# Optimization experiments

Hardware: AMD Instinct MI355X
Metric: run time of the kernel (lower is better)

The kernel has to match this reference:

```python
import jax, jax.numpy as jnp
import numpy as np

S = 64.0
M = 0.5
EPS = 1e-07
NORM_EPS = 1e-12  # matches torch F.normalize default eps
B, D, C = 512, 512, 64000


def _l2_normalize(a, axis=-1):
    n = jnp.sqrt(jnp.sum(a * a, axis=axis, keepdims=True))
    return a / jnp.maximum(n, NORM_EPS)


def setup_inputs() -> dict:
    key = jax.random.key(0)
    kx, ky, kw = jax.random.split(key, 3)
    x = jax.random.normal(kx, (B, D), dtype=jnp.float32)
    y = jax.random.randint(ky, (B,), 0, C, dtype=jnp.int64)
    # kaiming_uniform-ish init: bound = sqrt(6 / fan_in)
    bound = np.sqrt(6.0 / D).astype(np.float32)
    W = jax.random.uniform(kw, (C, D), dtype=jnp.float32, minval=-bound, maxval=bound)
    return {"x": x, "y": y, "W": W}


def reference(x, y, W):
    # cosine similarities: [B, C]
    theta = _l2_normalize(x) @ _l2_normalize(W).T
    # target logit per row
    tgt = jnp.take_along_axis(theta, y[:, None], axis=1)[:, 0]  # [B]
    numerator = S * jnp.cos(jnp.arccos(jnp.clip(tgt, -1.0 + EPS, 1.0 - EPS)) + M)
    # sum of exp(s*theta) over non-target classes (mask out target column)
    is_tgt = jnp.arange(C, dtype=y.dtype)[None, :] == y[:, None]  # [B, C]
    excl_sum = jnp.sum(jnp.where(is_tgt, 0.0, jnp.exp(S * theta)), axis=1)  # [B]
    denominator = jnp.exp(numerator) + excl_sum
    return -jnp.mean(numerator - jnp.log(denominator))
```

## Files before the change

### kernel.cpp

```cpp
#include <hip/hip_runtime.h>


#define B_N 512
#define D_N 512
#define C_N 64000
#define S_SCALE 64.0f
#define MARGIN 0.5f
#define EPS_C 1e-7f

typedef unsigned short ushort_t;
typedef __attribute__((ext_vector_type(8))) short short8;
typedef __attribute__((ext_vector_type(4))) float floatx4;

__device__ __forceinline__ ushort_t f2bf(float f) {
    unsigned int u = __float_as_uint(f);
    u += 0x7fffu + ((u >> 16) & 1u);
    return (ushort_t)(u >> 16);
}

__global__ void prep_kernel(const float* __restrict__ W,
                            const float* __restrict__ x,
                            ushort_t* __restrict__ Wn,
                            ushort_t* __restrict__ xn,
                            float* __restrict__ rowsum) {
    int b = blockIdx.x;
    int t = threadIdx.x;
    if (b == 16128) {
        rowsum[t] = 0.0f;
        rowsum[t + 256] = 0.0f;
        return;
    }
    const float* src;
    ushort_t* dst;
    int row;
    if (b < 16000) {
        row = b * 4 + (t >> 6);
        src = W + (size_t)row * D_N;
        dst = Wn + (size_t)row * D_N;
    } else {
        row = (b - 16000) * 4 + (t >> 6);
        src = x + (size_t)row * D_N;
        dst = xn + (size_t)row * D_N;
    }
    int lane = t & 63;
    const float4* p = (const float4*)src;
    float4 v0 = p[lane];
    float4 v1 = p[lane + 64];
    float ss = v0.x*v0.x + v0.y*v0.y + v0.z*v0.z + v0.w*v0.w
             + v1.x*v1.x + v1.y*v1.y + v1.z*v1.z + v1.w*v1.w;
#pragma unroll
    for (int off = 32; off > 0; off >>= 1) ss += __shfl_xor(ss, off);
    float sc = 1.0f / fmaxf(sqrtf(ss), 1e-12f);
    uint2 o0, o1;
    o0.x = (unsigned)f2bf(v0.x*sc) | ((unsigned)f2bf(v0.y*sc) << 16);
    o0.y = (unsigned)f2bf(v0.z*sc) | ((unsigned)f2bf(v0.w*sc) << 16);
    o1.x = (unsigned)f2bf(v1.x*sc) | ((unsigned)f2bf(v1.y*sc) << 16);
    o1.y = (unsigned)f2bf(v1.z*sc) | ((unsigned)f2bf(v1.w*sc) << 16);
    *(uint2*)(dst + lane * 4)       = o0;
    *(uint2*)(dst + 256 + lane * 4) = o1;
}

__device__ __forceinline__ void g2lds16(const ushort_t* g, ushort_t* l) {
    __builtin_amdgcn_global_load_lds(
        (const __attribute__((address_space(1))) void*)g,
        (__attribute__((address_space(3))) void*)l, 16, 0, 0);
}

__global__ void gemm_arcface_kernel(const ushort_t* __restrict__ A,
                                    const ushort_t* __restrict__ Bm,
                                    const int* __restrict__ y,
                                    float* __restrict__ rowsum,
                                    float* __restrict__ tgt) {
    __shared__ ushort_t sA[2 * 128 * 32];
    __shared__ ushort_t sB[2 * 128 * 32];
    __shared__ float rowacc[128];

    int t    = threadIdx.x;
    int lane = t & 63;
    int w    = t >> 6;
    int wr   = w >> 1, wc = w & 1;
    int rm0  = blockIdx.x * 128;
    int cn0  = blockIdx.y * 128;

    if (t < 128) rowacc[t] = 0.0f;

    floatx4 acc[4][4];
#pragma unroll
    for (int i = 0; i < 4; i++)
#pragma unroll
        for (int j = 0; j < 4; j++) acc[i][j] = (floatx4){0.f, 0.f, 0.f, 0.f};

    const ushort_t* gA0 = A  + (size_t)(rm0 + (t >> 2)) * D_N + (t & 3) * 8;
    const ushort_t* gB0 = Bm + (size_t)(cn0 + (t >> 2)) * D_N + (t & 3) * 8;

    int lq = lane >> 4;
    int lc = lane & 15;
    int fragA_off = (wr * 64 + lc) * 32 + lq * 8;
    int fragB_off = (wc * 64 + lc) * 32 + lq * 8;

    g2lds16(gA0,            sA + t * 8);
    g2lds16(gA0 + 64 * D_N, sA + (t + 256) * 8);
    g2lds16(gB0,            sB + t * 8);
    g2lds16(gB0 + 64 * D_N, sB + (t + 256) * 8);
    __syncthreads();

    for (int k = 0; k < 16; ++k) {
        int cur = (k & 1) * 4096;
        if (k < 15) {
            int nxt = ((k + 1) & 1) * 4096;
            int kk  = (k + 1) * 32;
            g2lds16(gA0 + kk,            sA + nxt + t * 8);
            g2lds16(gA0 + 64 * D_N + kk, sA + nxt + (t + 256) * 8);
            g2lds16(gB0 + kk,            sB + nxt + t * 8);
            g2lds16(gB0 + 64 * D_N + kk, sB + nxt + (t + 256) * 8);
        }

        short8 af[4], bf[4];
#pragma unroll
        for (int tm = 0; tm < 4; tm++)
            af[tm] = *(const short8*)(sA + cur + fragA_off + tm * 512);
#pragma unroll
        for (int tn = 0; tn < 4; tn++)
            bf[tn] = *(const short8*)(sB + cur + fragB_off + tn * 512);
#pragma unroll
        for (int tm = 0; tm < 4; tm++)
#pragma unroll
            for (int tn = 0; tn < 4; tn++)
                acc[tm][tn] = __builtin_amdgcn_mfma_f32_16x16x32_bf16(
                    af[tm], bf[tn], acc[tm][tn], 0, 0, 0);
        __syncthreads();
    }

#pragma unroll
    for (int tm = 0; tm < 4; tm++) {
#pragma unroll
        for (int r = 0; r < 4; r++) {
            int lrow = wr * 64 + tm * 16 + lq * 4 + r;
            int grow = rm0 + lrow;
            int yv   = y[grow];
            float esum = 0.0f;
#pragma unroll
            for (int tn = 0; tn < 4; tn++) {
                int gcol = cn0 + wc * 64 + tn * 16 + lc;
                float theta = acc[tm][tn][r];
                if (gcol == yv) {
                    tgt[grow] = theta;
                } else {
                    esum += __expf(S_SCALE * theta);
                }
            }
#pragma unroll
            for (int off = 1; off < 16; off <<= 1) esum += __shfl_xor(esum, off);
            if (lc == 0) atomicAdd(&rowacc[lrow], esum);
        }
    }
    __syncthreads();
    if (t < 128) atomicAdd(&rowsum[rm0 + t], rowacc[t]);
}

__global__ void finalize_kernel(const float* __restrict__ rowsum,
                                const float* __restrict__ tgt,
                                float* __restrict__ out) {
    __shared__ float red[256];
    int t = threadIdx.x;
    float s = 0.0f;
    for (int r = t; r < B_N; r += 256) {
        float tv = tgt[r];
        tv = fminf(fmaxf(tv, -1.0f + EPS_C), 1.0f - EPS_C);
        float num = S_SCALE * cosf(acosf(tv) + MARGIN);
        float den = expf(num) + rowsum[r];
        s += num - logf(den);
    }
    red[t] = s;
    __syncthreads();
    for (int o = 128; o > 0; o >>= 1) {
        if (t < o) red[t] += red[t + o];
        __syncthreads();
    }
    if (t == 0) out[0] = -red[0] / (float)B_N;
}

extern "C" void kernel_launch(void* const* d_in, const int* in_sizes, int n_in,
                              void* d_out, int out_size, void* d_ws, size_t ws_size,
                              hipStream_t stream) {
    const float* x = (const float*)d_in[0];
    const int*   y = (const int*)d_in[1];
    const float* W = (const float*)d_in[2];
    float* out = (float*)d_out;

    char* ws = (char*)d_ws;
    ushort_t* xn = (ushort_t*)ws;
    ushort_t* Wn = (ushort_t*)(ws + 524288);
    float* rowsum = (float*)(ws + 524288 + (size_t)C_N * D_N * 2);
    float* tgt    = rowsum + B_N;

    prep_kernel<<<16129, 256, 0, stream>>>(W, x, Wn, xn, rowsum);
    dim3 grid(4, C_N / 128);
    gemm_arcface_kernel<<<grid, 256, 0, stream>>>(xn, Wn, y, rowsum, tgt);
    finalize_kernel<<<1, 256, 0, stream>>>(rowsum, tgt, out);
}
```

Baseline: 256.0 us.

## Fuse W normalization into GEMM with full-K W tile resident in LDS

W row normalization and bf16 conversion now happen inside the GEMM kernel. Each 512-thread block normalizes 64 W rows into a swizzled LDS buffer covering the full K dimension, then streams all 512 normalized x rows against them. This removes the 64 MB bf16 Wn write and re-read and the separate large prep pass over W, leaving a single fp32 read of W. In exchange each block uses roughly 128 KB of LDS, which lowers occupancy, and shared x tiles are re-streamed from L2 by every block.

Result: slower. 269.4 us (+5.2%).

```diff
diff --git a/kernel.cpp b/kernel.cpp
--- a/kernel.cpp
+++ b/kernel.cpp
@@ -18,32 +18,19 @@
     return (ushort_t)(u >> 16);
 }
 
-__global__ void prep_kernel(const float* __restrict__ W,
-                            const float* __restrict__ x,
-                            ushort_t* __restrict__ Wn,
-                            ushort_t* __restrict__ xn,
-                            float* __restrict__ rowsum) {
+__global__ void xprep_kernel(const float* __restrict__ x,
+                             ushort_t* __restrict__ xn,
+                             float* __restrict__ rowsum) {
     int b = blockIdx.x;
     int t = threadIdx.x;
-    if (b == 16128) {
+    if (b == 128) {
         rowsum[t] = 0.0f;
         rowsum[t + 256] = 0.0f;
         return;
     }
-    const float* src;
-    ushort_t* dst;
-    int row;
-    if (b < 16000) {
-        row = b * 4 + (t >> 6);
-        src = W + (size_t)row * D_N;
-        dst = Wn + (size_t)row * D_N;
-    } else {
-        row = (b - 16000) * 4 + (t >> 6);
-        src = x + (size_t)row * D_N;
-        dst = xn + (size_t)row * D_N;
-    }
+    int row  = b * 4 + (t >> 6);
     int lane = t & 63;
-    const float4* p = (const float4*)src;
+    const float4* p = (const float4*)(x + (size_t)row * D_N);
     float4 v0 = p[lane];
     float4 v1 = p[lane + 64];
     float ss = v0.x*v0.x + v0.y*v0.y + v0.z*v0.z + v0.w*v0.w
@@ -51,6 +38,7 @@
 #pragma unroll
     for (int off = 32; off > 0; off >>= 1) ss += __shfl_xor(ss, off);
     float sc = 1.0f / fmaxf(sqrtf(ss), 1e-12f);
+    ushort_t* dst = xn + (size_t)row * D_N;
     uint2 o0, o1;
     o0.x = (unsigned)f2bf(v0.x*sc) | ((unsigned)f2bf(v0.y*sc) << 16);
     o0.y = (unsigned)f2bf(v0.z*sc) | ((unsigned)f2bf(v0.w*sc) << 16);
@@ -66,23 +54,48 @@
         (__attribute__((address_space(3))) void*)l, 16, 0, 0);
 }
 
-__global__ void gemm_arcface_kernel(const ushort_t* __restrict__ A,
-                                    const ushort_t* __restrict__ Bm,
-                                    const int* __restrict__ y,
-                                    float* __restrict__ rowsum,
-                                    float* __restrict__ tgt) {
-    __shared__ ushort_t sA[2 * 128 * 32];
-    __shared__ ushort_t sB[2 * 128 * 32];
-    __shared__ float rowacc[128];
+__global__ __launch_bounds__(512, 2)
+void gemm_fused_kernel(const float* __restrict__ W,
+                       const ushort_t* __restrict__ xn,
+                       const int* __restrict__ y,
+                       float* __restrict__ rowsum,
+                       float* __restrict__ tgt) {
+    __shared__ ushort_t sW[64 * 512];
+    __shared__ ushort_t sA[2 * 512 * 32];
 
     int t    = threadIdx.x;
     int lane = t & 63;
     int w    = t >> 6;
-    int wr   = w >> 1, wc = w & 1;
-    int rm0  = blockIdx.x * 128;
-    int cn0  = blockIdx.y * 128;
-
-    if (t < 128) rowacc[t] = 0.0f;
+    int lq   = lane >> 4;
+    int lc   = lane & 15;
+    int cn0  = blockIdx.x * 64;
+
+#pragma unroll
+    for (int rr = 0; rr < 8; ++rr) {
+        int row = w * 8 + rr;
+        const float4* p = (const float4*)(W + (size_t)(cn0 + row) * D_N);
+        float4 a = p[lane * 2];
+        float4 b = p[lane * 2 + 1];
+        float ss = a.x*a.x + a.y*a.y + a.z*a.z + a.w*a.w
+                 + b.x*b.x + b.y*b.y + b.z*b.z + b.w*b.w;
+#pragma unroll
+        for (int off = 32; off > 0; off >>= 1) ss += __shfl_xor(ss, off);
+        float sc = 1.0f / fmaxf(sqrtf(ss), 1e-12f);
+        uint4 o;
+        o.x = (unsigned)f2bf(a.x*sc) | ((unsigned)f2bf(a.y*sc) << 16);
+        o.y = (unsigned)f2bf(a.z*sc) | ((unsigned)f2bf(a.w*sc) << 16);
+        o.z = (unsigned)f2bf(b.x*sc) | ((unsigned)f2bf(b.y*sc) << 16);
+        o.w = (unsigned)f2bf(b.z*sc) | ((unsigned)f2bf(b.w*sc) << 16);
+        int kc = lane;
+        int rs = row ^ (kc & 7);
+        *((uint4*)(sW + kc * 512 + rs * 8)) = o;
+    }
+
+    const ushort_t* gA = xn + (size_t)(t >> 2) * D_N + (t & 3) * 8;
+#pragma unroll
+    for (int c = 0; c < 4; ++c)
+        g2lds16(gA + (size_t)c * 128 * D_N, sA + (t + c * 512) * 8);
+    __syncthreads();
 
     floatx4 acc[4][4];
 #pragma unroll
@@ -90,72 +103,62 @@
 #pragma unroll
         for (int j = 0; j < 4; j++) acc[i][j] = (floatx4){0.f, 0.f, 0.f, 0.f};
 
-    const ushort_t* gA0 = A  + (size_t)(rm0 + (t >> 2)) * D_N + (t & 3) * 8;
-    const ushort_t* gB0 = Bm + (size_t)(cn0 + (t >> 2)) * D_N + (t & 3) * 8;
-
-    int lq = lane >> 4;
-    int lc = lane & 15;
-    int fragA_off = (wr * 64 + lc) * 32 + lq * 8;
-    int fragB_off = (wc * 64 + lc) * 32 + lq * 8;
-
-    g2lds16(gA0,            sA + t * 8);
-    g2lds16(gA0 + 64 * D_N, sA + (t + 256) * 8);
-    g2lds16(gB0,            sB + t * 8);
-    g2lds16(gB0 + 64 * D_N, sB + (t + 256) * 8);
-    __syncthreads();
+    int fragA_base = (w * 64 + lc) * 32 + lq * 8;
 
     for (int k = 0; k < 16; ++k) {
-        int cur = (k & 1) * 4096;
+        int cur = (k & 1) * 16384;
         if (k < 15) {
-            int nxt = ((k + 1) & 1) * 4096;
+            int nxt = ((k + 1) & 1) * 16384;
             int kk  = (k + 1) * 32;
-            g2lds16(gA0 + kk,            sA + nxt + t * 8);
-            g2lds16(gA0 + 64 * D_N + kk, sA + nxt + (t + 256) * 8);
-            g2lds16(gB0 + kk,            sB + nxt + t * 8);
-            g2lds16(gB0 + 64 * D_N + kk, sB + nxt + (t + 256) * 8);
+#pragma unroll
+            for (int c = 0; c < 4; ++c)
+                g2lds16(gA + (size_t)c * 128 * D_N + kk,
+                        sA + nxt + (t + c * 512) * 8);
         }
-
-        short8 af[4], bf[4];
+        short8 af[4], bfr[4];
 #pragma unroll
         for (int tm = 0; tm < 4; tm++)
-            af[tm] = *(const short8*)(sA + cur + fragA_off + tm * 512);
-#pragma unroll
-        for (int tn = 0; tn < 4; tn++)
-            bf[tn] = *(const short8*)(sB + cur + fragB_off + tn * 512);
+            af[tm] = *(const short8*)(sA + cur + fragA_base + tm * 512);
+#pragma unroll
+        for (int tn = 0; tn < 4; tn++) {
+            int kc = k * 4 + lq;
+            int rs = (tn * 16 + lc) ^ (kc & 7);
+            bfr[tn] = *(const short8*)(sW + kc * 512 + rs * 8);
+        }
 #pragma unroll
         for (int tm = 0; tm < 4; tm++)
 #pragma unroll
             for (int tn = 0; tn < 4; tn++)
                 acc[tm][tn] = __builtin_amdgcn_mfma_f32_16x16x32_bf16(
-                    af[tm], bf[tn], acc[tm][tn], 0, 0, 0);
+                    af[tm], bfr[tn], acc[tm][tn], 0, 0, 0);
         __syncthreads();
     }
 
+    float* rowacc = (float*)sA;
 #pragma unroll
     for (int tm = 0; tm < 4; tm++) {
 #pragma unroll
         for (int r = 0; r < 4; r++) {
-            int lrow = wr * 64 + tm * 16 + lq * 4 + r;
-            int grow = rm0 + lrow;
-            int yv   = y[grow];
+            int lrow = w * 64 + tm * 16 + lq * 4 + r;
+            int yv   = y[lrow];
             float esum = 0.0f;
 #pragma unroll
             for (int tn = 0; tn < 4; tn++) {
-                int gcol = cn0 + wc * 64 + tn * 16 + lc;
+                int gcol = cn0 + tn * 16 + lc;
                 float theta = acc[tm][tn][r];
                 if (gcol == yv) {
-                    tgt[grow] = theta;
+                    tgt[lrow] = theta;
                 } else {
                     esum += __expf(S_SCALE * theta);
                 }
             }
 #pragma unroll
             for (int off = 1; off < 16; off <<= 1) esum += __shfl_xor(esum, off);
-            if (lc == 0) atomicAdd(&rowacc[lrow], esum);
+            if (lc == 0) rowacc[lrow] = esum;
         }
     }
     __syncthreads();
-    if (t < 128) atomicAdd(&rowsum[rm0 + t], rowacc[t]);
+    atomicAdd(&rowsum[t], rowacc[t]);
 }
 
 __global__ void finalize_kernel(const float* __restrict__ rowsum,
@@ -190,12 +193,10 @@
 
     char* ws = (char*)d_ws;
     ushort_t* xn = (ushort_t*)ws;
-    ushort_t* Wn = (ushort_t*)(ws + 524288);
-    float* rowsum = (float*)(ws + 524288 + (size_t)C_N * D_N * 2);
+    float* rowsum = (float*)(ws + 524288);
     float* tgt    = rowsum + B_N;
 
-    prep_kernel<<<16129, 256, 0, stream>>>(W, x, Wn, xn, rowsum);
-    dim3 grid(4, C_N / 128);
-    gemm_arcface_kernel<<<grid, 256, 0, stream>>>(xn, Wn, y, rowsum, tgt);
+    xprep_kernel<<<129, 256, 0, stream>>>(x, xn, rowsum);
+    gemm_fused_kernel<<<C_N / 64, 512, 0, stream>>>(W, xn, y, rowsum, tgt);
     finalize_kernel<<<1, 256, 0, stream>>>(rowsum, tgt, out);
 }
```
